# Performance work log

Hardware: AMD Instinct MI355X
Metric: run time of the kernel (lower is better)

## Reference

```python
import jax, jax.numpy as jnp
import numpy as np

B, DM, NH, NL, NP = 4, 768, 12, 3, 4
HD = DM // NH
H_IMG, W_IMG = 896, 896
LEVELS = [(H_IMG // 8, W_IMG // 8), (H_IMG // 16, W_IMG // 16), (H_IMG // 32, W_IMG // 32)]
QH, QW = H_IMG // 14, W_IMG // 14
LQ = QH * QW            # 4096 query tokens (stride-14 ViT grid)
LIN = sum(h * w for h, w in LEVELS)  # 16464 multi-scale value tokens


def setup_inputs() -> dict:
    key = jax.random.key(0)
    ks = jax.random.split(key, 14)
    s = 0.02
    return {
        "query": jax.random.normal(ks[0], (B, LQ, DM), jnp.float32),
        "feat": jax.random.normal(ks[1], (B, LIN, DM), jnp.float32),
        "ln_q_g": jnp.ones((DM,), jnp.float32),
        "ln_q_b": jnp.zeros((DM,), jnp.float32),
        "ln_f_g": jnp.ones((DM,), jnp.float32),
        "ln_f_b": jnp.zeros((DM,), jnp.float32),
        "W_off": jax.random.normal(ks[2], (DM, NH * NL * NP * 2), jnp.float32) * s,
        "b_off": jax.random.normal(ks[3], (NH * NL * NP * 2,), jnp.float32) * s,
        "W_attn": jax.random.normal(ks[4], (DM, NH * NL * NP), jnp.float32) * s,
        "b_attn": jax.random.normal(ks[5], (NH * NL * NP,), jnp.float32) * s,
        "W_val": jax.random.normal(ks[6], (DM, DM), jnp.float32) * s,
        "b_val": jnp.zeros((DM,), jnp.float32),
        "W_out": jax.random.normal(ks[7], (DM, DM), jnp.float32) * s,
        "b_out": jnp.zeros((DM,), jnp.float32),
        "gamma": jax.random.normal(ks[8], (DM,), jnp.float32) * s,
    }


def _ln(x, g, b, eps=1e-6):
    m = x.mean(-1, keepdims=True)
    v = ((x - m) ** 2).mean(-1, keepdims=True)
    return (x - m) * jax.lax.rsqrt(v + eps) * g + b


def _ref_points():
    # get_reference_points for the stride-14 query grid; pixel-center coords normalized
    ry, rx = jnp.meshgrid(
        (jnp.arange(QH, dtype=jnp.float32) + 0.5) / QH,
        (jnp.arange(QW, dtype=jnp.float32) + 0.5) / QW,
        indexing="ij",
    )
    return jnp.stack([rx.reshape(-1), ry.reshape(-1)], -1)  # (LQ, 2) in (x, y)


def _sample_level(v, loc, h_, w_):
    # v: (B, h_, w_, NH, HD); loc: (B, LQ, NH, NP, 2) normalized [0,1]
    # torch grid_sample bilinear, align_corners=False, zero padding
    x = loc[..., 0] * w_ - 0.5
    y = loc[..., 1] * h_ - 0.5
    x0 = jnp.floor(x)
    y0 = jnp.floor(y)
    wx = (x - x0)[..., None]
    wy = (y - y0)[..., None]
    x0i = x0.astype(jnp.int32)
    y0i = y0.astype(jnp.int32)
    bi = jnp.arange(B)[:, None, None, None]
    hi = jnp.arange(NH)[None, None, :, None]

    def g(yi, xi):
        valid = ((xi >= 0) & (xi < w_) & (yi >= 0) & (yi < h_)).astype(v.dtype)
        got = v[bi, jnp.clip(yi, 0, h_ - 1), jnp.clip(xi, 0, w_ - 1), hi]  # (B,LQ,NH,NP,HD)
        return got * valid[..., None]

    v00 = g(y0i, x0i)
    v01 = g(y0i, x0i + 1)
    v10 = g(y0i + 1, x0i)
    v11 = g(y0i + 1, x0i + 1)
    return v00 * (1 - wx) * (1 - wy) + v01 * wx * (1 - wy) + v10 * (1 - wx) * wy + v11 * wx * wy


def _injector(query, feat, ln_q_g, ln_q_b, ln_f_g, ln_f_b, W_off, b_off, W_attn, b_attn,
              W_val, b_val, W_out, b_out, gamma):
    q = _ln(query, ln_q_g, ln_q_b)
    f = _ln(feat, ln_f_g, ln_f_b)
    value = (f @ W_val + b_val).reshape(B, LIN, NH, HD)
    off = (q @ W_off + b_off).reshape(B, LQ, NH, NL, NP, 2)
    aw = jax.nn.softmax((q @ W_attn + b_attn).reshape(B, LQ, NH, NL * NP), axis=-1)
    aw = aw.reshape(B, LQ, NH, NL, NP)
    ref = _ref_points()  # (LQ, 2)
    offset_norm = jnp.array([[w, h] for h, w in LEVELS], jnp.float32)  # (NL, 2) = (W_, H_)
    loc = ref[None, :, None, None, None, :] + off / offset_norm[None, None, None, :, None, :]
    outs = []
    start = 0
    for lvl, (h_, w_) in enumerate(LEVELS):
        v = value[:, start:start + h_ * w_].reshape(B, h_, w_, NH, HD)
        outs.append(_sample_level(v, loc[:, :, :, lvl], h_, w_))
        start += h_ * w_
    samp = jnp.stack(outs, axis=3)  # (B, LQ, NH, NL, NP, HD)
    attn_out = (samp * aw[..., None]).sum(axis=(3, 4)).reshape(B, LQ, DM)
    attn_out = attn_out @ W_out + b_out
    return query + gamma * attn_out


def reference(query, feat, ln_q_g, ln_q_b, ln_f_g, ln_f_b, W_off, b_off, W_attn, b_attn,
              W_val, b_val, W_out, b_out, gamma):
    return _injector(query, feat, ln_q_g, ln_q_b, ln_f_g, ln_f_b, W_off, b_off, W_attn,
                     b_attn, W_val, b_val, W_out, b_out, gamma)
```

## Files before the change

### kernel.cpp

```cpp
#include <hip/hip_runtime.h>
#include <hip/hip_bf16.h>

typedef __hip_bfloat16 bf16;

#define BB    4
#define LQ    4096
#define LIN   16464
#define DM    768
#define NH    12
#define HD    64
#define K_DIM 768

typedef __attribute__((ext_vector_type(8))) __bf16 bfrag;
typedef __attribute__((ext_vector_type(4))) float  ffrag;

__device__ __forceinline__ void g2l16(const void* g, void* l) {
    __builtin_amdgcn_global_load_lds(
        (const __attribute__((address_space(1))) void*)g,
        (__attribute__((address_space(3))) void*)l, 16, 0, 0);
}

__device__ __forceinline__ int xcd_swz(int orig, int nwg) {
    int xcd = orig & 7, within = orig >> 3;
    int q = nwg >> 3, r = nwg & 7;
    return (xcd < r ? xcd * (q + 1) : r * (q + 1) + (xcd - r) * q) + within;
}

__global__ __launch_bounds__(256) void ln_kernel(
    const float* __restrict__ x, const float* __restrict__ g,
    const float* __restrict__ beta, bf16* __restrict__ y)
{
    int r = blockIdx.x * 4 + (threadIdx.x >> 6);
    int lane = threadIdx.x & 63;
    const float4* xr = (const float4*)(x + (size_t)r * DM);
    float4 v[3];
    #pragma unroll
    for (int i = 0; i < 3; i++) v[i] = xr[lane + 64 * i];
    float s = 0.f, ss = 0.f;
    #pragma unroll
    for (int i = 0; i < 3; i++) {
        s  += v[i].x + v[i].y + v[i].z + v[i].w;
        ss += v[i].x * v[i].x + v[i].y * v[i].y + v[i].z * v[i].z + v[i].w * v[i].w;
    }
    #pragma unroll
    for (int m = 1; m <= 32; m <<= 1) {
        s  += __shfl_xor(s, m);
        ss += __shfl_xor(ss, m);
    }
    float mean = s * (1.f / DM);
    float inv  = rsqrtf(ss * (1.f / DM) - mean * mean + 1e-6f);
    bf16* yr = y + (size_t)r * DM;
    #pragma unroll
    for (int i = 0; i < 3; i++) {
        float4 gg = ((const float4*)g)[lane + 64 * i];
        float4 bb = ((const float4*)beta)[lane + 64 * i];
        union { bf16 h[4]; uint2 u; } p;
        p.h[0] = __float2bfloat16((v[i].x - mean) * inv * gg.x + bb.x);
        p.h[1] = __float2bfloat16((v[i].y - mean) * inv * gg.y + bb.y);
        p.h[2] = __float2bfloat16((v[i].z - mean) * inv * gg.z + bb.z);
        p.h[3] = __float2bfloat16((v[i].w - mean) * inv * gg.w + bb.w);
        *(uint2*)(yr + (lane + 64 * i) * 4) = p.u;
    }
}

__global__ __launch_bounds__(256) void cast_transpose(
    const float* __restrict__ W, bf16* __restrict__ Wt, int N)
{
    __shared__ float t[32][33];
    int n0 = blockIdx.x * 32, k0 = blockIdx.y * 32;
    int tx = threadIdx.x & 31, ty = threadIdx.x >> 5;
    #pragma unroll
    for (int i = 0; i < 4; i++) {
        int k = k0 + ty + i * 8;
        int n = n0 + tx;
        t[ty + i * 8][tx] = (n < N) ? W[(size_t)k * N + n] : 0.f;
    }
    __syncthreads();
    #pragma unroll
    for (int i = 0; i < 4; i++) {
        int n = n0 + ty + i * 8;
        Wt[(size_t)n * K_DIM + k0 + tx] = __float2bfloat16(t[tx][ty + i * 8]);
    }
}

__global__ __launch_bounds__(512, 4) void gemm_value(
    const bf16*  __restrict__ A,
    const bf16*  __restrict__ Bt,
    const float* __restrict__ bias,
    bf16*        __restrict__ C,
    int M, int N)
{
    __shared__ __align__(16) char lds[73728];

    int tid  = threadIdx.x;
    int lane = tid & 63;
    int wave = tid >> 6;

    int nwg  = gridDim.x * gridDim.y;
    int orig = blockIdx.y * gridDim.x + blockIdx.x;
    int wg   = xcd_swz(orig, nwg);
    int bn = (wg % gridDim.x) * 128;
    int bm = (wg / gridDim.x) * 256;

    int ahalf = wave >> 2;
    int wc    = (wave & 3) * 32;

    int mrow = lane & 15;
    int kqs  = (((lane >> 4) ^ ((mrow >> 1) & 3)) * 8);

    ffrag acc[8][2] = {};

    int rA = tid >> 2;
    int kb = (((tid & 3) ^ ((rA >> 1) & 3)) * 8);
    int ra0 = min(bm + rA, M - 1), ra1 = min(bm + 128 + rA, M - 1);
    const bf16* gA0 = A  + (size_t)ra0 * K_DIM + kb;
    const bf16* gA1 = A  + (size_t)ra1 * K_DIM + kb;
    const bf16* gB0 = Bt + (size_t)(bn + rA) * K_DIM + kb;

    auto stage = [&](char* buf, int kt) {
        const int ko = kt * 32;
        g2l16(gA0 + ko, buf + tid * 16);
        g2l16(gA1 + ko, buf + tid * 16 + 8192);
        g2l16(gB0 + ko, buf + 16384 + tid * 16);
    };

    char* b0 = lds;
    char* b1 = lds + 24576;
    char* b2 = lds + 49152;
    stage(b0, 0); stage(b1, 1); stage(b2, 2);

    #pragma unroll
    for (int kt = 0; kt < 24; kt++) {
        if (kt + 2 < 24)      asm volatile("s_waitcnt vmcnt(6)" ::: "memory");
        else if (kt + 1 < 24) asm volatile("s_waitcnt vmcnt(3)" ::: "memory");
        else                  asm volatile("s_waitcnt vmcnt(0)" ::: "memory");
        __builtin_amdgcn_s_barrier();

        const char* Ab = b0 + (ahalf * 128) * 64;
        const char* Bb = b0 + 16384 + wc * 64;
        bfrag af[8], bf[2];
        #pragma unroll
        for (int mr = 0; mr < 8; mr++)
            af[mr] = *(const bfrag*)(Ab + (mr * 16 + mrow) * 64 + kqs * 2);
        #pragma unroll
        for (int nc = 0; nc < 2; nc++)
            bf[nc] = *(const bfrag*)(Bb + (nc * 16 + mrow) * 64 + kqs * 2);

        __builtin_amdgcn_s_setprio(1);
        #pragma unroll
        for (int mr = 0; mr < 8; mr++)
            #pragma unroll
            for (int nc = 0; nc < 2; nc++)
                acc[mr][nc] = __builtin_amdgcn_mfma_f32_16x16x32_bf16(
                    af[mr], bf[nc], acc[mr][nc], 0, 0, 0);
        __builtin_amdgcn_s_setprio(0);

        __builtin_amdgcn_s_barrier();
        if (kt + 3 < 24) stage(b0, kt + 3);
        char* tp = b0; b0 = b1; b1 = b2; b2 = tp;
    }

    int q4 = (lane >> 4) * 4;
    #pragma unroll
    for (int mr = 0; mr < 8; mr++) {
        #pragma unroll
        for (int rr = 0; rr < 4; rr++) {
            int rg = bm + ahalf * 128 + mr * 16 + q4 + rr;
            if (rg < M) {
                #pragma unroll
                for (int nc = 0; nc < 2; nc++) {
                    int cg = bn + wc + nc * 16 + mrow;
                    C[(size_t)rg * N + cg] =
                        __float2bfloat16(acc[mr][nc][rr] + bias[cg]);
                }
            }
        }
    }
}

__device__ __forceinline__ void gemm128_body(
    const bf16*  __restrict__ A,
    const bf16*  __restrict__ Bt,
    const float* __restrict__ bias,
    void*        __restrict__ C,
    const float* __restrict__ resid,
    const float* __restrict__ gamma,
    const float* __restrict__ bias2,
    int M, int N, int mode, int nsplit, char* lds)
{
    int tid  = threadIdx.x;
    int lane = tid & 63;

    int nwg  = gridDim.x * gridDim.y;
    int orig = blockIdx.y * gridDim.x + blockIdx.x;
    int wg = xcd_swz(orig, nwg);
    int bn = (wg % gridDim.x) * 128;
    int bm = (wg / gridDim.x) * 128;

    int wave = tid >> 6;
    int wr = (wave & 1) * 64, wc = (wave >> 1) * 64;

    ffrag acc[4][4] = {};

    int rA = tid >> 2;
    int kb = (((tid & 3) ^ ((rA >> 1) & 3)) * 8);
    int ra0 = min(bm + rA, M - 1), ra1 = min(bm + 64 + rA, M - 1);
    const bf16* gA0 = A  + (size_t)ra0 * K_DIM + kb;
    const bf16* gA1 = A  + (size_t)ra1 * K_DIM + kb;
    const bf16* gB0 = Bt + (size_t)(bn + rA) * K_DIM + kb;
    const bf16* gB1 = Bt + (size_t)(bn + 64 + rA) * K_DIM + kb;

    int mrow = lane & 15;
    int kqs  = (((lane >> 4) ^ ((mrow >> 1) & 3)) * 8);

    auto stage = [&](char* buf, int kt) {
        const int ko = kt * 32;
        g2l16(gA0 + ko, buf + tid * 16);
        g2l16(gA1 + ko, buf + tid * 16 + 4096);
        g2l16(gB0 + ko, buf + 8192 + tid * 16);
        g2l16(gB1 + ko, buf + 8192 + tid * 16 + 4096);
    };

    stage(lds, 0);
    asm volatile("s_waitcnt vmcnt(0)" ::: "memory");
    __builtin_amdgcn_s_barrier();

    #pragma unroll
    for (int kt = 0; kt < 24; kt++) {
        char* cur = lds + (kt & 1) * 16384;
        char* nxt = lds + ((kt & 1) ^ 1) * 16384;
        if (kt + 1 < 24) stage(nxt, kt + 1);

        bfrag a[4], b[4];
        #pragma unroll
        for (int t = 0; t < 4; t++) {
            a[t] = *(const bfrag*)(cur + ((wr + t * 16 + mrow) * 32 + kqs) * 2);
            b[t] = *(const bfrag*)(cur + 8192 + ((wc + t * 16 + mrow) * 32 + kqs) * 2);
        }
        __builtin_amdgcn_s_setprio(1);
        #pragma unroll
        for (int i = 0; i < 4; i++)
            #pragma unroll
            for (int j = 0; j < 4; j++)
                acc[i][j] = __builtin_amdgcn_mfma_f32_16x16x32_bf16(
                    a[i], b[j], acc[i][j], 0, 0, 0);
        __builtin_amdgcn_s_setprio(0);

        asm volatile("s_waitcnt vmcnt(0)" ::: "memory");
        __builtin_amdgcn_s_barrier();
    }

    int q4 = (lane >> 4) * 4;
    #pragma unroll
    for (int i = 0; i < 4; i++) {
        #pragma unroll
        for (int rr = 0; rr < 4; rr++) {
            int rg = bm + wr + i * 16 + q4 + rr;
            if (rg < M) {
                #pragma unroll
                for (int j = 0; j < 4; j++) {
                    int cg = bn + wc + j * 16 + mrow;
                    if (cg < N) {
                        float bv = (mode == 3 && cg >= nsplit) ? bias2[cg - nsplit]
                                                               : bias[cg];
                        float v = acc[i][j][rr] + bv;
                        size_t idx = (size_t)rg * N + cg;
                        if (mode == 2)      ((float*)C)[idx] = resid[idx] + gamma[cg] * v;
                        else                ((float*)C)[idx] = v;
                    }
                }
            }
        }
    }
}

__global__ __launch_bounds__(256) void gemm128_comb(
    const bf16* __restrict__ A, const bf16* __restrict__ Bt,
    const float* __restrict__ bias, void* __restrict__ C,
    const float* __restrict__ bias2, int M, int N, int nsplit)
{
    __shared__ __align__(16) char lds[32768];
    gemm128_body(A, Bt, bias, C, nullptr, nullptr, bias2, M, N, 3, nsplit, lds);
}

__global__ __launch_bounds__(256) void gemm128_out(
    const bf16* __restrict__ A, const bf16* __restrict__ Bt,
    const float* __restrict__ bias, void* __restrict__ C,
    const float* __restrict__ resid, const float* __restrict__ gamma,
    int M, int N)
{
    __shared__ __align__(16) char lds[32768];
    gemm128_body(A, Bt, bias, C, resid, gamma, nullptr, M, N, 2, 0, lds);
}

__global__ __launch_bounds__(256) void prep_kernel(
    const float* __restrict__ comb, uint4* __restrict__ pre)
{
    int t  = blockIdx.x * 256 + threadIdx.x;
    int p  = t % 12;
    int uh = t / 12;
    int h  = uh % NH;
    int bq = uh / NH;
    int q  = bq & (LQ - 1);
    int b  = bq >> 12;

    const float* rowp = comb + (size_t)bq * 432;
    const float* lg = rowp + 288 + h * 12;

    float4 a4 = ((const float4*)lg)[0];
    float4 b4 = ((const float4*)lg)[1];
    float4 c4 = ((const float4*)lg)[2];
    float mx = fmaxf(fmaxf(fmaxf(fmaxf(a4.x, a4.y), fmaxf(a4.z, a4.w)),
                           fmaxf(fmaxf(b4.x, b4.y), fmaxf(b4.z, b4.w))),
                     fmaxf(fmaxf(c4.x, c4.y), fmaxf(c4.z, c4.w)));
    float den = __expf(a4.x - mx) + __expf(a4.y - mx) + __expf(a4.z - mx) +
                __expf(a4.w - mx) + __expf(b4.x - mx) + __expf(b4.y - mx) +
                __expf(b4.z - mx) + __expf(b4.w - mx) + __expf(c4.x - mx) +
                __expf(c4.y - mx) + __expf(c4.z - mx) + __expf(c4.w - mx);
    float lp  = lg[p];
    float awn = __expf(lp - mx) / den;

    int lvl = p >> 2;
    const int wl = (lvl == 0) ? 112 : (lvl == 1 ? 56 : 28);
    const int sl = (lvl == 0) ? 0   : (lvl == 1 ? 12544 : 15680);

    float2 oxy = *(const float2*)(rowp + h * 24 + p * 2);

    float rx = ((q & 63) + 0.5f) * (1.f / 64.f);
    float ry = ((q >> 6) + 0.5f) * (1.f / 64.f);
    float x = rx * wl + oxy.x - 0.5f;
    float y = ry * wl + oxy.y - 0.5f;
    float xf = floorf(x), yf = floorf(y);
    float wx = x - xf, wy = y - yf;
    int x0 = (int)xf, x1 = x0 + 1;
    int y0 = (int)yf, y1 = y0 + 1;
    bool vx0 = (unsigned)x0 < (unsigned)wl, vx1 = (unsigned)x1 < (unsigned)wl;
    bool vy0 = (unsigned)y0 < (unsigned)wl, vy1 = (unsigned)y1 < (unsigned)wl;
    int x0c = min(max(x0, 0), wl - 1), x1c = min(max(x1, 0), wl - 1);
    int y0c = min(max(y0, 0), wl - 1), y1c = min(max(y1, 0), wl - 1);

    int base = b * LIN + sl;
    int yb0 = (base + y0c * wl) * (NH * HD) + h * HD;
    int yb1 = (base + y1c * wl) * (NH * HD) + h * HD;
    int xb0 = x0c * (NH * HD);
    int xb1 = x1c * (NH * HD);

    float wx0 = vx0 ? (1.f - wx) * awn : 0.f;
    float wx1 = vx1 ? wx * awn : 0.f;
    float wy0f = vy0 ? (1.f - wy) : 0.f;
    float wy1f = vy1 ? wy : 0.f;

    uint4 r0 = {(unsigned)(yb0 + xb0), __float_as_uint(wx0 * wy0f),
                (unsigned)(yb0 + xb1), __float_as_uint(wx1 * wy0f)};
    uint4 r1 = {(unsigned)(yb1 + xb0), __float_as_uint(wx0 * wy1f),
                (unsigned)(yb1 + xb1), __float_as_uint(wx1 * wy1f)};
    pre[(size_t)t * 2 + 0] = r0;
    pre[(size_t)t * 2 + 1] = r1;
}

__global__ __launch_bounds__(256) void sample_kernel(
    const bf16*  __restrict__ value,
    const uint4* __restrict__ pre,
    bf16*        __restrict__ attn)
{
    __shared__ float red[4][8][64];

    int wv   = threadIdx.x >> 6;
    int wg   = xcd_swz(blockIdx.x, gridDim.x);
    int unit = __builtin_amdgcn_readfirstlane((wg << 2) + wv);
    int lane = threadIdx.x & 63;
    int o   = lane & 7;
    int c8  = lane >> 3;
    int k   = c8 & 3;
    int hi  = (c8 >> 2) & 1;
    int h  = unit % NH;
    int bq = unit / NH;

    const uint2* pr = (const uint2*)((const char*)pre
        + (size_t)unit * 384 + hi * 32 + k * 8);

    uint2 rec[6];
    #pragma unroll
    for (int it = 0; it < 6; it++) rec[it] = pr[it * 8];

    const bf16* vb = value + o * 8;
    uint4 v[6];
    #pragma unroll
    for (int it = 0; it < 6; it++)
        v[it] = *(const uint4*)(vb + (int)rec[it].x);

    float acc[8] = {0.f};
    #pragma unroll
    for (int it = 0; it < 6; it++) {
        float w = __uint_as_float(rec[it].y);
        const unsigned* u = (const unsigned*)&v[it];
        #pragma unroll
        for (int j = 0; j < 4; j++) {
            float f0 = __uint_as_float(u[j] << 16);
            float f1 = __uint_as_float(u[j] & 0xFFFF0000u);
            acc[j * 2 + 0] = fmaf(w, f0, acc[j * 2 + 0]);
            acc[j * 2 + 1] = fmaf(w, f1, acc[j * 2 + 1]);
        }
    }

    {
        float* rw = &red[wv][c8][0];
        int base = (o * 8 + c8 * 4) & 63;
        *(float4*)&rw[base] = float4{acc[0], acc[1], acc[2], acc[3]};
        *(float4*)&rw[(base + 4) & 63] = float4{acc[4], acc[5], acc[6], acc[7]};
    }
    asm volatile("s_waitcnt lgkmcnt(0)" ::: "memory");
    __builtin_amdgcn_sched_barrier(0);
    float sum = 0.f;
    #pragma unroll
    for (int s = 0; s < 8; s++)
        sum += red[wv][s][(lane + s * 4) & 63];

    attn[(size_t)bq * DM + h * HD + lane] = __float2bfloat16(sum);
}

extern "C" void kernel_launch(void* const* d_in, const int* in_sizes, int n_in,
                              void* d_out, int out_size, void* d_ws, size_t ws_size,
                              hipStream_t stream)
{
    const float* query  = (const float*)d_in[0];
    const float* feat   = (const float*)d_in[1];
    const float* ln_q_g = (const float*)d_in[2];
    const float* ln_q_b = (const float*)d_in[3];
    const float* ln_f_g = (const float*)d_in[4];
    const float* ln_f_b = (const float*)d_in[5];
    const float* W_off  = (const float*)d_in[6];
    const float* b_off  = (const float*)d_in[7];
    const float* W_attn = (const float*)d_in[8];
    const float* b_attn = (const float*)d_in[9];
    const float* W_val  = (const float*)d_in[10];
    const float* b_val  = (const float*)d_in[11];
    const float* W_out  = (const float*)d_in[12];
    const float* b_out  = (const float*)d_in[13];
    const float* gamma  = (const float*)d_in[14];
    float* out = (float*)d_out;

    char* ws = (char*)d_ws;
    char* od = (char*)d_out;
    const int M_F = BB * LIN;
    const int M_Q = BB * LQ;

    bf16*  value  = (bf16*)(ws);
    bf16*  f_ln   = (bf16*)(ws + 101154816);
    bf16*  Wt_out = (bf16*)(ws + 101154816);
    uint4* pre    = (uint4*)(ws + 101154816 + 4194304);
    bf16*  q_ln   = (bf16*)(ws + 202309632);
    bf16*  attn   = (bf16*)(ws + 202309632);

    bf16*  Wt_val  = (bf16*)(od);
    bf16*  Wt_comb = (bf16*)(od + 1179648);
    float* comb    = (float*)(od + 2162688);

    cast_transpose<<<dim3(24, 24), 256, 0, stream>>>(W_val, Wt_val, 768);
    cast_transpose<<<dim3(9, 24), 256, 0, stream>>>(W_off, Wt_comb, 288);
    cast_transpose<<<dim3(7, 24), 256, 0, stream>>>(
        W_attn, Wt_comb + (size_t)288 * K_DIM, 144);

    ln_kernel<<<M_F / 4, 256, 0, stream>>>(feat, ln_f_g, ln_f_b, f_ln);
    ln_kernel<<<M_Q / 4, 256, 0, stream>>>(query, ln_q_g, ln_q_b, q_ln);

    gemm_value<<<dim3(6, (M_F + 255) / 256), 512, 0, stream>>>(
        f_ln, Wt_val, b_val, value, M_F, DM);

    cast_transpose<<<dim3(24, 24), 256, 0, stream>>>(W_out, Wt_out, 768);

    gemm128_comb<<<dim3(4, M_Q / 128), 256, 0, stream>>>(
        q_ln, Wt_comb, b_off, comb, b_attn, M_Q, 432, 288);

    prep_kernel<<<(M_Q * NH * 12) / 256, 256, 0, stream>>>(comb, pre);

    sample_kernel<<<(M_Q * NH) / 4, 256, 0, stream>>>(value, pre, attn);

    gemm128_out<<<dim3(6, M_Q / 128), 256, 0, stream>>>(
        attn, Wt_out, b_out, out, query, gamma, M_Q, DM);
}
```

Baseline: 678.3 us.

## Unify GEMMs on triple-buffered 256x128 pipelined kernel for comb and out projections

Turns the triple-buffered 256x128-tile, 512-thread value-projection GEMM into a template with MODE-specific epilogues. The offset/attention-logit GEMM and the output projection (residual plus gamma) now use it instead of the 128x128 double-buffered kernel that waited for all loads to finish every k-step. The aim is to overlap global-to-LDS loads with MFMA work and reuse more of each A tile on these two smaller GEMMs. In exchange it launches half as many workgroups, which lowers parallelism on an M=16384 problem and may leave CUs idle.

After: 663.6 us. 1.02x faster.

```diff
diff --git a/kernel.cpp b/kernel.cpp
--- a/kernel.cpp
+++ b/kernel.cpp
@@ -83,102 +83,8 @@
     }
 }
 
-__global__ __launch_bounds__(512, 4) void gemm_value(
-    const bf16*  __restrict__ A,
-    const bf16*  __restrict__ Bt,
-    const float* __restrict__ bias,
-    bf16*        __restrict__ C,
-    int M, int N)
-{
-    __shared__ __align__(16) char lds[73728];
-
-    int tid  = threadIdx.x;
-    int lane = tid & 63;
-    int wave = tid >> 6;
-
-    int nwg  = gridDim.x * gridDim.y;
-    int orig = blockIdx.y * gridDim.x + blockIdx.x;
-    int wg   = xcd_swz(orig, nwg);
-    int bn = (wg % gridDim.x) * 128;
-    int bm = (wg / gridDim.x) * 256;
-
-    int ahalf = wave >> 2;
-    int wc    = (wave & 3) * 32;
-
-    int mrow = lane & 15;
-    int kqs  = (((lane >> 4) ^ ((mrow >> 1) & 3)) * 8);
-
-    ffrag acc[8][2] = {};
-
-    int rA = tid >> 2;
-    int kb = (((tid & 3) ^ ((rA >> 1) & 3)) * 8);
-    int ra0 = min(bm + rA, M - 1), ra1 = min(bm + 128 + rA, M - 1);
-    const bf16* gA0 = A  + (size_t)ra0 * K_DIM + kb;
-    const bf16* gA1 = A  + (size_t)ra1 * K_DIM + kb;
-    const bf16* gB0 = Bt + (size_t)(bn + rA) * K_DIM + kb;
-
-    auto stage = [&](char* buf, int kt) {
-        const int ko = kt * 32;
-        g2l16(gA0 + ko, buf + tid * 16);
-        g2l16(gA1 + ko, buf + tid * 16 + 8192);
-        g2l16(gB0 + ko, buf + 16384 + tid * 16);
-    };
-
-    char* b0 = lds;
-    char* b1 = lds + 24576;
-    char* b2 = lds + 49152;
-    stage(b0, 0); stage(b1, 1); stage(b2, 2);
-
-    #pragma unroll
-    for (int kt = 0; kt < 24; kt++) {
-        if (kt + 2 < 24)      asm volatile("s_waitcnt vmcnt(6)" ::: "memory");
-        else if (kt + 1 < 24) asm volatile("s_waitcnt vmcnt(3)" ::: "memory");
-        else                  asm volatile("s_waitcnt vmcnt(0)" ::: "memory");
-        __builtin_amdgcn_s_barrier();
-
-        const char* Ab = b0 + (ahalf * 128) * 64;
-        const char* Bb = b0 + 16384 + wc * 64;
-        bfrag af[8], bf[2];
-        #pragma unroll
-        for (int mr = 0; mr < 8; mr++)
-            af[mr] = *(const bfrag*)(Ab + (mr * 16 + mrow) * 64 + kqs * 2);
-        #pragma unroll
-        for (int nc = 0; nc < 2; nc++)
-            bf[nc] = *(const bfrag*)(Bb + (nc * 16 + mrow) * 64 + kqs * 2);
-
-        __builtin_amdgcn_s_setprio(1);
-        #pragma unroll
-        for (int mr = 0; mr < 8; mr++)
-            #pragma unroll
-            for (int nc = 0; nc < 2; nc++)
-                acc[mr][nc] = __builtin_amdgcn_mfma_f32_16x16x32_bf16(
-                    af[mr], bf[nc], acc[mr][nc], 0, 0, 0);
-        __builtin_amdgcn_s_setprio(0);
-
-        __builtin_amdgcn_s_barrier();
-        if (kt + 3 < 24) stage(b0, kt + 3);
-        char* tp = b0; b0 = b1; b1 = b2; b2 = tp;
-    }
-
-    int q4 = (lane >> 4) * 4;
-    #pragma unroll
-    for (int mr = 0; mr < 8; mr++) {
-        #pragma unroll
-        for (int rr = 0; rr < 4; rr++) {
-            int rg = bm + ahalf * 128 + mr * 16 + q4 + rr;
-            if (rg < M) {
-                #pragma unroll
-                for (int nc = 0; nc < 2; nc++) {
-                    int cg = bn + wc + nc * 16 + mrow;
-                    C[(size_t)rg * N + cg] =
-                        __float2bfloat16(acc[mr][nc][rr] + bias[cg]);
-                }
-            }
-        }
-    }
-}
-
-__device__ __forceinline__ void gemm128_body(
+template<int MODE>
+__global__ __launch_bounds__(512, 4) void gemm_pipe(
     const bf16*  __restrict__ A,
     const bf16*  __restrict__ Bt,
     const float* __restrict__ bias,
@@ -186,111 +92,107 @@
     const float* __restrict__ resid,
     const float* __restrict__ gamma,
     const float* __restrict__ bias2,
-    int M, int N, int mode, int nsplit, char* lds)
-{
+    int M, int N_out, int nsplit)
+{
+    __shared__ __align__(16) char lds[73728];
+
     int tid  = threadIdx.x;
     int lane = tid & 63;
+    int wave = tid >> 6;
 
     int nwg  = gridDim.x * gridDim.y;
     int orig = blockIdx.y * gridDim.x + blockIdx.x;
-    int wg = xcd_swz(orig, nwg);
+    int wg   = xcd_swz(orig, nwg);
     int bn = (wg % gridDim.x) * 128;
-    int bm = (wg / gridDim.x) * 128;
-
-    int wave = tid >> 6;
-    int wr = (wave & 1) * 64, wc = (wave >> 1) * 64;
-
-    ffrag acc[4][4] = {};
+    int bm = (wg / gridDim.x) * 256;
+
+    int ahalf = wave >> 2;
+    int wc    = (wave & 3) * 32;
+
+    int mrow = lane & 15;
+    int kqs  = (((lane >> 4) ^ ((mrow >> 1) & 3)) * 8);
+
+    ffrag acc[8][2] = {};
 
     int rA = tid >> 2;
     int kb = (((tid & 3) ^ ((rA >> 1) & 3)) * 8);
-    int ra0 = min(bm + rA, M - 1), ra1 = min(bm + 64 + rA, M - 1);
+    int ra0 = min(bm + rA, M - 1), ra1 = min(bm + 128 + rA, M - 1);
     const bf16* gA0 = A  + (size_t)ra0 * K_DIM + kb;
     const bf16* gA1 = A  + (size_t)ra1 * K_DIM + kb;
     const bf16* gB0 = Bt + (size_t)(bn + rA) * K_DIM + kb;
-    const bf16* gB1 = Bt + (size_t)(bn + 64 + rA) * K_DIM + kb;
-
-    int mrow = lane & 15;
-    int kqs  = (((lane >> 4) ^ ((mrow >> 1) & 3)) * 8);
 
     auto stage = [&](char* buf, int kt) {
         const int ko = kt * 32;
         g2l16(gA0 + ko, buf + tid * 16);
-        g2l16(gA1 + ko, buf + tid * 16 + 4096);
-        g2l16(gB0 + ko, buf + 8192 + tid * 16);
-        g2l16(gB1 + ko, buf + 8192 + tid * 16 + 4096);
+        g2l16(gA1 + ko, buf + tid * 16 + 8192);
+        g2l16(gB0 + ko, buf + 16384 + tid * 16);
     };
 
-    stage(lds, 0);
-    asm volatile("s_waitcnt vmcnt(0)" ::: "memory");
-    __builtin_amdgcn_s_barrier();
+    char* b0 = lds;
+    char* b1 = lds + 24576;
+    char* b2 = lds + 49152;
+    stage(b0, 0); stage(b1, 1); stage(b2, 2);
 
     #pragma unroll
     for (int kt = 0; kt < 24; kt++) {
-        char* cur = lds + (kt & 1) * 16384;
-        char* nxt = lds + ((kt & 1) ^ 1) * 16384;
-        if (kt + 1 < 24) stage(nxt, kt + 1);
-
-        bfrag a[4], b[4];
-        #pragma unroll
-        for (int t = 0; t < 4; t++) {
-            a[t] = *(const bfrag*)(cur + ((wr + t * 16 + mrow) * 32 + kqs) * 2);
-            b[t] = *(const bfrag*)(cur + 8192 + ((wc + t * 16 + mrow) * 32 + kqs) * 2);
-        }
+        if (kt + 2 < 24)      asm volatile("s_waitcnt vmcnt(6)" ::: "memory");
+        else if (kt + 1 < 24) asm volatile("s_waitcnt vmcnt(3)" ::: "memory");
+        else                  asm volatile("s_waitcnt vmcnt(0)" ::: "memory");
+        __builtin_amdgcn_s_barrier();
+
+        const char* Ab = b0 + (ahalf * 128) * 64;
+        const char* Bb = b0 + 16384 + wc * 64;
+        bfrag af[8], bf[2];
+        #pragma unroll
+        for (int mr = 0; mr < 8; mr++)
+            af[mr] = *(const bfrag*)(Ab + (mr * 16 + mrow) * 64 + kqs * 2);
+        #pragma unroll
+        for (int nc = 0; nc < 2; nc++)
+            bf[nc] = *(const bfrag*)(Bb + (nc * 16 + mrow) * 64 + kqs * 2);
+
         __builtin_amdgcn_s_setprio(1);
         #pragma unroll
-        for (int i = 0; i < 4; i++)
+        for (int mr = 0; mr < 8; mr++)
             #pragma unroll
-            for (int j = 0; j < 4; j++)
-                acc[i][j] = __builtin_amdgcn_mfma_f32_16x16x32_bf16(
-                    a[i], b[j], acc[i][j], 0, 0, 0);
+            for (int nc = 0; nc < 2; nc++)
+                acc[mr][nc] = __builtin_amdgcn_mfma_f32_16x16x32_bf16(
+                    af[mr], bf[nc], acc[mr][nc], 0, 0, 0);
         __builtin_amdgcn_s_setprio(0);
 
-        asm volatile("s_waitcnt vmcnt(0)" ::: "memory");
         __builtin_amdgcn_s_barrier();
+        if (kt + 3 < 24) stage(b0, kt + 3);
+        char* tp = b0; b0 = b1; b1 = b2; b2 = tp;
     }
 
     int q4 = (lane >> 4) * 4;
     #pragma unroll
-    for (int i = 0; i < 4; i++) {
+    for (int mr = 0; mr < 8; mr++) {
         #pragma unroll
         for (int rr = 0; rr < 4; rr++) {
-            int rg = bm + wr + i * 16 + q4 + rr;
+            int rg = bm + ahalf * 128 + mr * 16 + q4 + rr;
             if (rg < M) {
                 #pragma unroll
-                for (int j = 0; j < 4; j++) {
-                    int cg = bn + wc + j * 16 + mrow;
-                    if (cg < N) {
-                        float bv = (mode == 3 && cg >= nsplit) ? bias2[cg - nsplit]
-                                                               : bias[cg];
-                        float v = acc[i][j][rr] + bv;
-                        size_t idx = (size_t)rg * N + cg;
-                        if (mode == 2)      ((float*)C)[idx] = resid[idx] + gamma[cg] * v;
-                        else                ((float*)C)[idx] = v;
+                for (int nc = 0; nc < 2; nc++) {
+                    int cg = bn + wc + nc * 16 + mrow;
+                    if (MODE == 0) {
+                        ((bf16*)C)[(size_t)rg * N_out + cg] =
+                            __float2bfloat16(acc[mr][nc][rr] + bias[cg]);
+                    } else if (MODE == 2) {
+                        size_t idx = (size_t)rg * N_out + cg;
+                        ((float*)C)[idx] = resid[idx] +
+                            gamma[cg] * (acc[mr][nc][rr] + bias[cg]);
+                    } else {
+                        if (cg < N_out) {
+                            float bv = (cg >= nsplit) ? bias2[cg - nsplit]
+                                                      : bias[cg];
+                            ((float*)C)[(size_t)rg * N_out + cg] =
+                                acc[mr][nc][rr] + bv;
+                        }
                     }
                 }
             }
         }
     }
-}
-
-__global__ __launch_bounds__(256) void gemm128_comb(
-    const bf16* __restrict__ A, const bf16* __restrict__ Bt,
-    const float* __restrict__ bias, void* __restrict__ C,
-    const float* __restrict__ bias2, int M, int N, int nsplit)
-{
-    __shared__ __align__(16) char lds[32768];
-    gemm128_body(A, Bt, bias, C, nullptr, nullptr, bias2, M, N, 3, nsplit, lds);
-}
-
-__global__ __launch_bounds__(256) void gemm128_out(
-    const bf16* __restrict__ A, const bf16* __restrict__ Bt,
-    const float* __restrict__ bias, void* __restrict__ C,
-    const float* __restrict__ resid, const float* __restrict__ gamma,
-    int M, int N)
-{
-    __shared__ __align__(16) char lds[32768];
-    gemm128_body(A, Bt, bias, C, resid, gamma, nullptr, M, N, 2, 0, lds);
 }
 
 __global__ __launch_bounds__(256) void prep_kernel(
@@ -464,18 +366,18 @@
     ln_kernel<<<M_F / 4, 256, 0, stream>>>(feat, ln_f_g, ln_f_b, f_ln);
     ln_kernel<<<M_Q / 4, 256, 0, stream>>>(query, ln_q_g, ln_q_b, q_ln);
 
-    gemm_value<<<dim3(6, (M_F + 255) / 256), 512, 0, stream>>>(
-        f_ln, Wt_val, b_val, value, M_F, DM);
+    gemm_pipe<0><<<dim3(6, (M_F + 255) / 256), 512, 0, stream>>>(
+        f_ln, Wt_val, b_val, value, nullptr, nullptr, nullptr, M_F, DM, 0);
 
     cast_transpose<<<dim3(24, 24), 256, 0, stream>>>(W_out, Wt_out, 768);
 
-    gemm128_comb<<<dim3(4, M_Q / 128), 256, 0, stream>>>(
-        q_ln, Wt_comb, b_off, comb, b_attn, M_Q, 432, 288);
+    gemm_pipe<3><<<dim3(4, M_Q / 256), 512, 0, stream>>>(
+        q_ln, Wt_comb, b_off, comb, nullptr, nullptr, b_attn, M_Q, 432, 288);
 
     prep_kernel<<<(M_Q * NH * 12) / 256, 256, 0, stream>>>(comb, pre);
 
     sample_kernel<<<(M_Q * NH) / 4, 256, 0, stream>>>(value, pre, attn);
 
-    gemm128_out<<<dim3(6, M_Q / 128), 256, 0, stream>>>(
-        attn, Wt_out, b_out, out, query, gamma, M_Q, DM);
-}
+    gemm_pipe<2><<<dim3(6, M_Q / 256), 512, 0, stream>>>(
+        attn, Wt_out, b_out, out, query, gamma, nullptr, M_Q, DM, 0);
+}
```
